# Kernel tuning notes

Measured on AMD Instinct MI355X. Metric: run time of the kernel, lower is better.

Reference implementation:

```python
import jax, jax.numpy as jnp
import numpy as np
import math

B, T, C = 1, 2048, 2048
N_HEAD = 32
N_QUERY_GROUPS = 8
HEAD_SIZE = 64
ROPE_N_ELEM = 16  # int(0.25 * 64)
Q_PER_KV = N_HEAD // N_QUERY_GROUPS  # 4
QKV_DIM = (N_HEAD + 2 * N_QUERY_GROUPS) * HEAD_SIZE  # 3072


def setup_inputs() -> dict:
    key = jax.random.key(0)
    ks = jax.random.split(key, 7)
    x = jax.random.normal(ks[0], (B, T, C), dtype=jnp.float32)
    # realistic rope tables
    inv_freq = 1.0 / (10000.0 ** (jnp.arange(0, ROPE_N_ELEM, 2, dtype=jnp.float32) / ROPE_N_ELEM))
    t = jnp.arange(T, dtype=jnp.float32)
    freqs = jnp.outer(t, inv_freq)                       # [T, rope/2]
    emb = jnp.concatenate([freqs, freqs], axis=-1)       # [T, rope]
    cos, sin = jnp.cos(emb), jnp.sin(emb)
    s = 0.02
    W_attn = jax.random.normal(ks[1], (QKV_DIM, C), dtype=jnp.float32) * s
    b_attn = jax.random.normal(ks[2], (QKV_DIM,), dtype=jnp.float32) * s
    W_proj = jax.random.normal(ks[3], (C, N_HEAD * HEAD_SIZE), dtype=jnp.float32) * s
    b_proj = jax.random.normal(ks[4], (C,), dtype=jnp.float32) * s
    return {"x": x, "cos": cos, "sin": sin, "W_attn": W_attn, "b_attn": b_attn,
            "W_proj": W_proj, "b_proj": b_proj}


def _apply_rope(t, cos, sin):
    # t: [B, H, T, rope]; cos/sin: [T, rope]
    half = t.shape[-1] // 2
    t1, t2 = t[..., :half], t[..., half:]
    rotated = jnp.concatenate([-t2, t1], axis=-1)
    return t * cos + rotated * sin


def reference(x, cos, sin, W_attn, b_attn, W_proj, b_proj):
    Bc, Tc, Cc = x.shape
    qkv = x @ W_attn.T + b_attn                                   # [B, T, 3072]
    qkv = qkv.reshape(Bc, Tc, N_QUERY_GROUPS, Q_PER_KV + 2, HEAD_SIZE)
    qkv = qkv.transpose(0, 2, 3, 1, 4)                            # [B, G, q_per_kv+2, T, hs]
    q = qkv[:, :, :Q_PER_KV]                                      # [B, G, q_per_kv, T, hs]
    k = qkv[:, :, Q_PER_KV:Q_PER_KV + 1]                          # [B, G, 1, T, hs]
    v = qkv[:, :, Q_PER_KV + 1:]
    # GQA expand (n_query_groups != n_head, prefill path)
    k = jnp.broadcast_to(k, (Bc, N_QUERY_GROUPS, Q_PER_KV, Tc, HEAD_SIZE))
    v = jnp.broadcast_to(v, (Bc, N_QUERY_GROUPS, Q_PER_KV, Tc, HEAD_SIZE))
    q = q.reshape(Bc, N_HEAD, Tc, HEAD_SIZE)
    k = k.reshape(Bc, N_HEAD, Tc, HEAD_SIZE)
    v = v.reshape(Bc, N_HEAD, Tc, HEAD_SIZE)
    # partial RoPE on first ROPE_N_ELEM dims
    q = jnp.concatenate([_apply_rope(q[..., :ROPE_N_ELEM], cos, sin), q[..., ROPE_N_ELEM:]], axis=-1)
    k = jnp.concatenate([_apply_rope(k[..., :ROPE_N_ELEM], cos, sin), k[..., ROPE_N_ELEM:]], axis=-1)
    # causal SDPA with scale 1/sqrt(head_size)
    scale = 1.0 / math.sqrt(HEAD_SIZE)
    scores = jnp.einsum('bhqd,bhkd->bhqk', q, k) * scale          # [B, H, T, T]
    causal = jnp.tril(jnp.ones((Tc, Tc), dtype=bool))
    scores = jnp.where(causal, scores, jnp.finfo(scores.dtype).min)
    attn = jax.nn.softmax(scores, axis=-1)
    y = jnp.einsum('bhqk,bhkd->bhqd', attn, v)                    # [B, H, T, hs]
    y = y.transpose(0, 2, 1, 3).reshape(Bc, Tc, N_HEAD * HEAD_SIZE)
    return y @ W_proj.T + b_proj
```

## Files before the change

kernel.cpp:

```cpp
#include <hip/hip_runtime.h>
#include <hip/hip_bf16.h>

using u16 = unsigned short;
typedef float f32x4 __attribute__((ext_vector_type(4)));
typedef __bf16 bf16x8 __attribute__((ext_vector_type(8)));

#define T_SEQ 2048
#define C_DIM 2048
#define QKV_DIM 3072
#define N_HEAD 32
#define N_GROUPS 8
#define HEAD_SIZE 64
#define ROPE_N 16
#define NEG_BIG (-1e30f)
#define LS 72
#define LSP 76
#define QSCALE 0.18033688011112043f

__device__ inline float bf2f(u16 u) {
    union { float f; unsigned v; } x; x.v = ((unsigned)u) << 16; return x.f;
}
__device__ inline u16 f2bf(float f) {
    __bf16 h = (__bf16)f;
    return *(u16*)&h;
}
__device__ inline int4 cvt8(int4 lo, int4 hi) {
    const float* fa = (const float*)&lo;
    const float* fb = (const float*)&hi;
    __attribute__((aligned(16))) u16 o[8] = {
        f2bf(fa[0]), f2bf(fa[1]), f2bf(fa[2]), f2bf(fa[3]),
        f2bf(fb[0]), f2bf(fb[1]), f2bf(fb[2]), f2bf(fb[3]) };
    return *(const int4*)o;
}

__device__ __forceinline__ int detect_fp32(const unsigned* __restrict__ xw) {
    int cnt = 0;
#pragma unroll
    for (int i = 0; i < 128; i++) {
        unsigned w = xw[i];
        cnt += (((w >> 7)  & 0xFF) >= 0xC0);
        cnt += (((w >> 23) & 0xFF) >= 0xC0);
    }
    return cnt > 8;
}

__device__ __forceinline__ void gl_lds16(const u16* g, u16* l) {
    __builtin_amdgcn_global_load_lds(
        (const __attribute__((address_space(1))) unsigned int*)g,
        (__attribute__((address_space(3))) unsigned int*)l,
        16, 0, 0);
}

struct ConvDesc {
    const void* src[7];
    u16*        dst[7];
    int         off8[8];
};

__global__ void convert_all(ConvDesc cd)
{
    const int fl = detect_fp32((const unsigned*)cd.src[0]);
    int gid = blockIdx.x * blockDim.x + threadIdx.x;
    if (gid >= cd.off8[7]) return;
    int seg = 0;
#pragma unroll
    for (int s = 1; s < 7; s++) seg += (gid >= cd.off8[s]);
    int i = (gid - cd.off8[seg]) * 8;
    if (fl) {
        const float4* s = (const float4*)((const float*)cd.src[seg] + i);
        *(int4*)(cd.dst[seg] + i) = cvt8(*(const int4*)&s[0], *(const int4*)&s[1]);
    } else {
        *(int4*)(cd.dst[seg] + i) = *(const int4*)((const u16*)cd.src[seg] + i);
    }
}

__global__ __launch_bounds__(256) void gemm_qkv_rope(
    const u16* __restrict__ A, const u16* __restrict__ W,
    const u16* __restrict__ bias,
    const u16* __restrict__ ccos, const u16* __restrict__ csin,
    u16* __restrict__ Qout, u16* __restrict__ Kout, u16* __restrict__ Vtout)
{
    __shared__ __attribute__((aligned(16))) u16 lds_a[2][64 * 64];
    __shared__ __attribute__((aligned(16))) u16 lds_b[2][128 * 64];

    const int tid  = threadIdx.x;
    const int wave = tid >> 6;
    const int lane = tid & 63;
    const int quad = lane >> 4;
    const int l16  = lane & 15;
    const int bm = blockIdx.y * 64;
    const int bn = blockIdx.x * 128;
    const int K = C_DIM;

    f32x4 acc[4][2] = {};

    int srow[4], sgc[4];
#pragma unroll
    for (int k = 0; k < 4; k++) {
        int s = tid + k * 256;
        srow[k] = s >> 3;
        sgc[k]  = (s & 7) ^ (srow[k] & 7);
    }
    const int xh = l16 & 7;

    auto stage = [&](int k0, int p) {
#pragma unroll
        for (int k = 0; k < 2; k++) {
            int s = tid + k * 256;
            gl_lds16(A + (size_t)(bm + srow[k]) * K + k0 + sgc[k] * 8, lds_a[p] + s * 8);
        }
#pragma unroll
        for (int k = 0; k < 4; k++) {
            int s = tid + k * 256;
            gl_lds16(W + (size_t)(bn + srow[k]) * K + k0 + sgc[k] * 8, lds_b[p] + s * 8);
        }
    };

    stage(0, 0);
    const int nsteps = K / 64;
    for (int kt = 0; kt < nsteps; kt++) {
        const int p = kt & 1;
        __syncthreads();
        if (kt + 1 < nsteps) stage((kt + 1) * 64, p ^ 1);

        bf16x8 afr[4][2], bfr[2][2];
#pragma unroll
        for (int ks = 0; ks < 2; ks++) {
            int c = ((ks * 4 + quad) ^ xh) * 8;
#pragma unroll
            for (int i = 0; i < 4; i++)
                afr[i][ks] = *(const bf16x8*)(lds_a[p] + (i * 16 + l16) * 64 + c);
#pragma unroll
            for (int j = 0; j < 2; j++)
                bfr[j][ks] = *(const bf16x8*)(lds_b[p] + (wave * 32 + j * 16 + l16) * 64 + c);
        }
#pragma unroll
        for (int ks = 0; ks < 2; ks++)
#pragma unroll
            for (int i = 0; i < 4; i++)
#pragma unroll
                for (int j = 0; j < 2; j++)
                    acc[i][j] = __builtin_amdgcn_mfma_f32_16x16x32_bf16(afr[i][ks], bfr[j][ks], acc[i][j], 0, 0, 0);
    }

#pragma unroll
    for (int j = 0; j < 2; j++) {
        const int colb = bn + wave * 32 + j * 16;
        const int col  = colb + l16;
        const int slot = (colb % 384) >> 6;
        const int g    = colb / 384;
        const int dbase = colb & 63;
        const int d    = dbase + l16;
        const float bv = bf2f(bias[col]);
        const bool rope = (dbase == 0) && (slot != 5);
#pragma unroll
        for (int i = 0; i < 4; i++) {
            const int trow = bm + i * 16 + quad * 4;
#pragma unroll
            for (int r = 0; r < 4; r++) {
                float v = acc[i][j][r] + bv;
                float outv = v;
                if (rope) {
                    float part = __shfl_xor(v, 8, 64);
                    float rot = (l16 < 8) ? -part : part;
                    float cc = bf2f(ccos[(trow + r) * ROPE_N + l16]);
                    float ss = bf2f(csin[(trow + r) * ROPE_N + l16]);
                    outv = v * cc + rot * ss;
                }
                const int t = trow + r;
                if (slot < 4) {
                    int hh = g * 4 + slot;
                    Qout[((size_t)hh * T_SEQ + t) * 64 + d] = f2bf(outv * QSCALE);
                } else if (slot == 4) {
                    Kout[((size_t)g * T_SEQ + t) * 64 + d] = f2bf(outv);
                } else {
                    Vtout[((size_t)g * 64 + d) * T_SEQ + t] = f2bf(outv);
                }
            }
        }
    }
}

__global__ __launch_bounds__(256) void gemm_bt(
    const u16* __restrict__ A, const u16* __restrict__ W,
    const u16* __restrict__ bias, u16* __restrict__ Cout,
    int M, int N, int K, const unsigned* __restrict__ xprobe)
{
    __shared__ __attribute__((aligned(16))) u16 lds_a[2][64 * 64];
    __shared__ __attribute__((aligned(16))) u16 lds_b[2][64 * 64];

    const int tid  = threadIdx.x;
    const int wave = tid >> 6;
    const int lane = tid & 63;
    const int quad = lane >> 4;
    const int l16  = lane & 15;
    const int bm = blockIdx.y * 64;
    const int bn = blockIdx.x * 64;
    const int fl = detect_fp32(xprobe);

    f32x4 acc[4] = {};

    int srow[2], sgc[2];
#pragma unroll
    for (int k = 0; k < 2; k++) {
        int s = tid + k * 256;
        srow[k] = s >> 3;
        sgc[k]  = (s & 7) ^ (srow[k] & 7);
    }
    const int xh = l16 & 7;

    auto stage = [&](int k0, int p) {
#pragma unroll
        for (int k = 0; k < 2; k++) {
            int s = tid + k * 256;
            gl_lds16(A + (size_t)(bm + srow[k]) * K + k0 + sgc[k] * 8, lds_a[p] + s * 8);
            gl_lds16(W + (size_t)(bn + srow[k]) * K + k0 + sgc[k] * 8, lds_b[p] + s * 8);
        }
    };

    stage(0, 0);
    const int nsteps = K / 64;
    for (int kt = 0; kt < nsteps; kt++) {
        const int p = kt & 1;
        __syncthreads();
        if (kt + 1 < nsteps) stage((kt + 1) * 64, p ^ 1);

        bf16x8 afr[4][2], bfr[2];
#pragma unroll
        for (int ks = 0; ks < 2; ks++) {
            int c = ((ks * 4 + quad) ^ xh) * 8;
#pragma unroll
            for (int i = 0; i < 4; i++)
                afr[i][ks] = *(const bf16x8*)(lds_a[p] + (i * 16 + l16) * 64 + c);
            bfr[ks] = *(const bf16x8*)(lds_b[p] + (wave * 16 + l16) * 64 + c);
        }
#pragma unroll
        for (int ks = 0; ks < 2; ks++)
#pragma unroll
            for (int i = 0; i < 4; i++)
                acc[i] = __builtin_amdgcn_mfma_f32_16x16x32_bf16(afr[i][ks], bfr[ks], acc[i], 0, 0, 0);
    }

    const int col = bn + wave * 16 + l16;
    const float bv = bf2f(bias[col]);
#pragma unroll
    for (int i = 0; i < 4; i++) {
        int row = bm + i * 16 + quad * 4;
#pragma unroll
        for (int r = 0; r < 4; r++) {
            float v = acc[i][r] + bv;
            size_t idx = (size_t)(row + r) * N + col;
            if (fl) ((float*)Cout)[idx] = v;
            else    Cout[idx] = f2bf(v);
        }
    }
}

__global__ __launch_bounds__(256) void flash_attn(
    const u16* __restrict__ Q, const u16* __restrict__ K,
    const u16* __restrict__ Vt, u16* __restrict__ Y)
{
    __shared__ __attribute__((aligned(16))) u16 lds_q[64 * LS];
    __shared__ __attribute__((aligned(16))) u16 lds_k[2][64 * LS];
    __shared__ __attribute__((aligned(16))) u16 lds_vt[2][64 * LS];
    __shared__ __attribute__((aligned(16))) u16 lds_p[4][16 * LSP];

    const int h  = blockIdx.y;
    const int g  = h >> 2;
    const int tid  = threadIdx.x;
    const int wave = tid >> 6;
    const int lane = tid & 63;
    const int quad = lane >> 4;
    const int l16  = lane & 15;
    const int NQT = T_SEQ / 64;

    const u16* Qh = Q  + (size_t)h * T_SEQ * 64;
    const u16* Kg = K  + (size_t)g * T_SEQ * 64;
    const u16* Vg = Vt + (size_t)g * 64 * T_SEQ;

    const int srow = tid >> 3, scc = (tid & 7) * 8;

    bf16x8 vones;
#pragma unroll
    for (int i = 0; i < 8; i++) vones[i] = (__bf16)1.0f;

    int4 kr0, kr1, vr0, vr1;
    auto load_tile = [&](int k0) {
        kr0 = *(const int4*)(Kg + (size_t)(k0 + srow) * 64 + scc);
        kr1 = *(const int4*)(Kg + (size_t)(k0 + srow + 32) * 64 + scc);
        vr0 = *(const int4*)(Vg + (size_t)srow * T_SEQ + k0 + scc);
        vr1 = *(const int4*)(Vg + (size_t)(srow + 32) * T_SEQ + k0 + scc);
    };

    for (int pass = 0; pass < 2; pass++) {
        const int qt = pass ? (NQT - 1 - blockIdx.x) : blockIdx.x;
        const int q0 = qt * 64;

        __syncthreads();
        for (int s = tid; s < 512; s += 256) {
            int row = s >> 3, cc = (s & 7) * 8;
            *(int4*)(lds_q + row * LS + cc) =
                *(const int4*)(Qh + (size_t)(q0 + row) * 64 + cc);
        }
        __syncthreads();

        bf16x8 a_q[2];
#pragma unroll
        for (int ks = 0; ks < 2; ks++)
            a_q[ks] = *(const bf16x8*)(lds_q + (wave * 16 + l16) * LS + ks * 32 + quad * 8);

        f32x4 o_acc[4] = {};
        f32x4 acc_l = {};

        load_tile(0);

        for (int kt = 0; kt <= qt; kt++) {
            const int p = kt & 1;
            *(int4*)(lds_k[p]  + srow * LS + scc)        = kr0;
            *(int4*)(lds_k[p]  + (srow + 32) * LS + scc) = kr1;
            *(int4*)(lds_vt[p] + srow * LS + scc)        = vr0;
            *(int4*)(lds_vt[p] + (srow + 32) * LS + scc) = vr1;
            __syncthreads();
            if (kt < qt) load_tile((kt + 1) * 64);

            f32x4 sc[4] = {};
#pragma unroll
            for (int ks = 0; ks < 2; ks++)
#pragma unroll
                for (int t = 0; t < 4; t++) {
                    bf16x8 bk = *(const bf16x8*)(lds_k[p] + (t * 16 + l16) * LS + ks * 32 + quad * 8);
                    sc[t] = __builtin_amdgcn_mfma_f32_16x16x32_bf16(a_q[ks], bk, sc[t], 0, 0, 0);
                }

            if (kt == qt) {
                const int row_g = q0 + wave * 16 + quad * 4;
                const int k0 = kt * 64;
#pragma unroll
                for (int t = 0; t < 4; t++) {
                    int col_g = k0 + t * 16 + l16;
#pragma unroll
                    for (int r = 0; r < 4; r++)
                        if (col_g > row_g + r) sc[t][r] = NEG_BIG;
                }
            }

#pragma unroll
            for (int t = 0; t < 4; t++) {
                int colo = t * 16 + l16;
#pragma unroll
                for (int r = 0; r < 4; r++) {
                    float pv = __builtin_amdgcn_exp2f(sc[t][r]);
                    lds_p[wave][(quad * 4 + r) * LSP + colo] = f2bf(pv);
                }
            }

#pragma unroll
            for (int ks = 0; ks < 2; ks++) {
                bf16x8 apf = *(const bf16x8*)(lds_p[wave] + l16 * LSP + ks * 32 + quad * 8);
#pragma unroll
                for (int t = 0; t < 4; t++) {
                    bf16x8 bvf = *(const bf16x8*)(lds_vt[p] + (t * 16 + l16) * LS + ks * 32 + quad * 8);
                    o_acc[t] = __builtin_amdgcn_mfma_f32_16x16x32_bf16(apf, bvf, o_acc[t], 0, 0, 0);
                }
                acc_l = __builtin_amdgcn_mfma_f32_16x16x32_bf16(apf, vones, acc_l, 0, 0, 0);
            }
        }

#pragma unroll
        for (int t = 0; t < 4; t++)
#pragma unroll
            for (int r = 0; r < 4; r++) {
                int row = q0 + wave * 16 + quad * 4 + r;
                int d   = t * 16 + l16;
                Y[(size_t)row * (N_HEAD * HEAD_SIZE) + h * 64 + d] = f2bf(o_acc[t][r] / acc_l[r]);
            }
    }
}

extern "C" void kernel_launch(void* const* d_in, const int* in_sizes, int n_in,
                              void* d_out, int out_size, void* d_ws, size_t ws_size,
                              hipStream_t stream)
{
    u16* base = (u16*)d_ws;

    u16* cx   = base;
    u16* cWa  = cx  + (size_t)T_SEQ * C_DIM;
    u16* cba  = cWa + (size_t)QKV_DIM * C_DIM;
    u16* cWp  = cba + QKV_DIM;
    u16* cbp  = cWp + (size_t)C_DIM * C_DIM;
    u16* ccos = cbp + C_DIM;
    u16* csin = ccos + (size_t)T_SEQ * ROPE_N;
    u16* Qb   = csin + (size_t)T_SEQ * ROPE_N;
    u16* Kb   = Qb + (size_t)N_HEAD * T_SEQ * HEAD_SIZE;
    u16* Vtb  = Kb + (size_t)N_GROUPS * T_SEQ * HEAD_SIZE;
    u16* Yb   = Vtb + (size_t)N_GROUPS * T_SEQ * HEAD_SIZE;

    dim3 blk(256);

    ConvDesc cd;
    const int sizes[7] = { T_SEQ * C_DIM, T_SEQ * ROPE_N, T_SEQ * ROPE_N,
                           QKV_DIM * C_DIM, QKV_DIM, C_DIM * C_DIM, C_DIM };
    u16* dsts[7] = { cx, ccos, csin, cWa, cba, cWp, cbp };
    int acc8 = 0;
    for (int i = 0; i < 7; i++) {
        cd.src[i] = d_in[i];
        cd.dst[i] = dsts[i];
        cd.off8[i] = acc8;
        acc8 += sizes[i] / 8;
    }
    cd.off8[7] = acc8;
    convert_all<<<dim3((acc8 + 255) / 256), blk, 0, stream>>>(cd);

    gemm_qkv_rope<<<dim3(QKV_DIM / 128, T_SEQ / 64), blk, 0, stream>>>(
        cx, cWa, cba, ccos, csin, Qb, Kb, Vtb);
    flash_attn<<<dim3(T_SEQ / 128, N_HEAD), blk, 0, stream>>>(Qb, Kb, Vtb, Yb);
    gemm_bt<<<dim3(C_DIM / 64, T_SEQ / 64), blk, 0, stream>>>(
        Yb, cWp, cbp, (u16*)d_out, T_SEQ, C_DIM, N_HEAD * HEAD_SIZE,
        (const unsigned*)d_in[0]);
}
```

Measured before the change: 251.0 us.

## Use direct global-to-LDS async loads with XOR swizzle in flash attention

The flash attention kernel now stages Q, K and V tiles straight into shared memory with a gl_lds16 helper (presumably defined in the hidden part of the file) instead of going through registers. Padded rows are replaced by an XOR-swizzled layout to avoid bank conflicts. The two-pass causal pairing per block becomes one query tile per block, launched longest-first over twice as many blocks. This aims to cut register pressure and load latency, at the cost of losing the paired load balancing, and it depends on the async LDS load semantics and barrier placement being correct.

```diff
diff --git a/kernel.cpp b/kernel.cpp
--- a/kernel.cpp
+++ b/kernel.cpp
@@ -13,7 +13,6 @@
 #define HEAD_SIZE 64
 #define ROPE_N 16
 #define NEG_BIG (-1e30f)
-#define LS 72
 #define LSP 76
 #define QSCALE 0.18033688011112043f
 
@@ -260,121 +259,125 @@
     const u16* __restrict__ Q, const u16* __restrict__ K,
     const u16* __restrict__ Vt, u16* __restrict__ Y)
 {
-    __shared__ __attribute__((aligned(16))) u16 lds_q[64 * LS];
-    __shared__ __attribute__((aligned(16))) u16 lds_k[2][64 * LS];
-    __shared__ __attribute__((aligned(16))) u16 lds_vt[2][64 * LS];
+    __shared__ __attribute__((aligned(16))) u16 lds_q[64 * 64];
+    __shared__ __attribute__((aligned(16))) u16 lds_k[2][64 * 64];
+    __shared__ __attribute__((aligned(16))) u16 lds_vt[2][64 * 64];
     __shared__ __attribute__((aligned(16))) u16 lds_p[4][16 * LSP];
 
     const int h  = blockIdx.y;
     const int g  = h >> 2;
+    const int qt = 31 - blockIdx.x;
+    const int q0 = qt * 64;
     const int tid  = threadIdx.x;
     const int wave = tid >> 6;
     const int lane = tid & 63;
     const int quad = lane >> 4;
     const int l16  = lane & 15;
-    const int NQT = T_SEQ / 64;
 
     const u16* Qh = Q  + (size_t)h * T_SEQ * 64;
     const u16* Kg = K  + (size_t)g * T_SEQ * 64;
     const u16* Vg = Vt + (size_t)g * 64 * T_SEQ;
 
-    const int srow = tid >> 3, scc = (tid & 7) * 8;
+    int srow[2], sgc[2];
+#pragma unroll
+    for (int k = 0; k < 2; k++) {
+        int s = tid + k * 256;
+        srow[k] = s >> 3;
+        sgc[k]  = (s & 7) ^ (srow[k] & 7);
+    }
+    const int xh = l16 & 7;
 
     bf16x8 vones;
 #pragma unroll
     for (int i = 0; i < 8; i++) vones[i] = (__bf16)1.0f;
 
-    int4 kr0, kr1, vr0, vr1;
-    auto load_tile = [&](int k0) {
-        kr0 = *(const int4*)(Kg + (size_t)(k0 + srow) * 64 + scc);
-        kr1 = *(const int4*)(Kg + (size_t)(k0 + srow + 32) * 64 + scc);
-        vr0 = *(const int4*)(Vg + (size_t)srow * T_SEQ + k0 + scc);
-        vr1 = *(const int4*)(Vg + (size_t)(srow + 32) * T_SEQ + k0 + scc);
+    auto stage = [&](int k0, int p) {
+#pragma unroll
+        for (int k = 0; k < 2; k++) {
+            int s = tid + k * 256;
+            gl_lds16(Kg + (size_t)(k0 + srow[k]) * 64 + sgc[k] * 8, lds_k[p] + s * 8);
+            gl_lds16(Vg + (size_t)srow[k] * T_SEQ + k0 + sgc[k] * 8, lds_vt[p] + s * 8);
+        }
     };
 
-    for (int pass = 0; pass < 2; pass++) {
-        const int qt = pass ? (NQT - 1 - blockIdx.x) : blockIdx.x;
-        const int q0 = qt * 64;
-
+#pragma unroll
+    for (int k = 0; k < 2; k++) {
+        int s = tid + k * 256;
+        gl_lds16(Qh + (size_t)(q0 + srow[k]) * 64 + sgc[k] * 8, lds_q + s * 8);
+    }
+    stage(0, 0);
+
+    f32x4 o_acc[4] = {};
+    f32x4 acc_l = {};
+    bf16x8 a_q[2];
+    bool q_loaded = false;
+
+    for (int kt = 0; kt <= qt; kt++) {
+        const int p = kt & 1;
         __syncthreads();
-        for (int s = tid; s < 512; s += 256) {
-            int row = s >> 3, cc = (s & 7) * 8;
-            *(int4*)(lds_q + row * LS + cc) =
-                *(const int4*)(Qh + (size_t)(q0 + row) * 64 + cc);
-        }
-        __syncthreads();
-
-        bf16x8 a_q[2];
-#pragma unroll
-        for (int ks = 0; ks < 2; ks++)
-            a_q[ks] = *(const bf16x8*)(lds_q + (wave * 16 + l16) * LS + ks * 32 + quad * 8);
-
-        f32x4 o_acc[4] = {};
-        f32x4 acc_l = {};
-
-        load_tile(0);
-
-        for (int kt = 0; kt <= qt; kt++) {
-            const int p = kt & 1;
-            *(int4*)(lds_k[p]  + srow * LS + scc)        = kr0;
-            *(int4*)(lds_k[p]  + (srow + 32) * LS + scc) = kr1;
-            *(int4*)(lds_vt[p] + srow * LS + scc)        = vr0;
-            *(int4*)(lds_vt[p] + (srow + 32) * LS + scc) = vr1;
-            __syncthreads();
-            if (kt < qt) load_tile((kt + 1) * 64);
-
-            f32x4 sc[4] = {};
+        if (kt < qt) stage((kt + 1) * 64, p ^ 1);
+
+        if (!q_loaded) {
 #pragma unroll
             for (int ks = 0; ks < 2; ks++)
-#pragma unroll
-                for (int t = 0; t < 4; t++) {
-                    bf16x8 bk = *(const bf16x8*)(lds_k[p] + (t * 16 + l16) * LS + ks * 32 + quad * 8);
-                    sc[t] = __builtin_amdgcn_mfma_f32_16x16x32_bf16(a_q[ks], bk, sc[t], 0, 0, 0);
-                }
-
-            if (kt == qt) {
-                const int row_g = q0 + wave * 16 + quad * 4;
-                const int k0 = kt * 64;
-#pragma unroll
-                for (int t = 0; t < 4; t++) {
-                    int col_g = k0 + t * 16 + l16;
-#pragma unroll
-                    for (int r = 0; r < 4; r++)
-                        if (col_g > row_g + r) sc[t][r] = NEG_BIG;
-                }
+                a_q[ks] = *(const bf16x8*)(lds_q + (wave * 16 + l16) * 64 + (((ks * 4 + quad) ^ xh) * 8));
+            q_loaded = true;
+        }
+
+        f32x4 sc[4] = {};
+#pragma unroll
+        for (int ks = 0; ks < 2; ks++) {
+            int c = ((ks * 4 + quad) ^ xh) * 8;
+#pragma unroll
+            for (int t = 0; t < 4; t++) {
+                bf16x8 bk = *(const bf16x8*)(lds_k[p] + (t * 16 + l16) * 64 + c);
+                sc[t] = __builtin_amdgcn_mfma_f32_16x16x32_bf16(a_q[ks], bk, sc[t], 0, 0, 0);
             }
-
+        }
+
+        if (kt == qt) {
+            const int row_g = q0 + wave * 16 + quad * 4;
+            const int k0 = kt * 64;
 #pragma unroll
             for (int t = 0; t < 4; t++) {
-                int colo = t * 16 + l16;
-#pragma unroll
-                for (int r = 0; r < 4; r++) {
-                    float pv = __builtin_amdgcn_exp2f(sc[t][r]);
-                    lds_p[wave][(quad * 4 + r) * LSP + colo] = f2bf(pv);
-                }
+                int col_g = k0 + t * 16 + l16;
+#pragma unroll
+                for (int r = 0; r < 4; r++)
+                    if (col_g > row_g + r) sc[t][r] = NEG_BIG;
             }
-
-#pragma unroll
-            for (int ks = 0; ks < 2; ks++) {
-                bf16x8 apf = *(const bf16x8*)(lds_p[wave] + l16 * LSP + ks * 32 + quad * 8);
-#pragma unroll
-                for (int t = 0; t < 4; t++) {
-                    bf16x8 bvf = *(const bf16x8*)(lds_vt[p] + (t * 16 + l16) * LS + ks * 32 + quad * 8);
-                    o_acc[t] = __builtin_amdgcn_mfma_f32_16x16x32_bf16(apf, bvf, o_acc[t], 0, 0, 0);
-                }
-                acc_l = __builtin_amdgcn_mfma_f32_16x16x32_bf16(apf, vones, acc_l, 0, 0, 0);
+        }
+
+#pragma unroll
+        for (int t = 0; t < 4; t++) {
+            int colo = t * 16 + l16;
+#pragma unroll
+            for (int r = 0; r < 4; r++) {
+                float pv = __builtin_amdgcn_exp2f(sc[t][r]);
+                lds_p[wave][(quad * 4 + r) * LSP + colo] = f2bf(pv);
             }
         }
 
 #pragma unroll
-        for (int t = 0; t < 4; t++)
-#pragma unroll
-            for (int r = 0; r < 4; r++) {
-                int row = q0 + wave * 16 + quad * 4 + r;
-                int d   = t * 16 + l16;
-                Y[(size_t)row * (N_HEAD * HEAD_SIZE) + h * 64 + d] = f2bf(o_acc[t][r] / acc_l[r]);
+        for (int ks = 0; ks < 2; ks++) {
+            int c = ((ks * 4 + quad) ^ xh) * 8;
+            bf16x8 apf = *(const bf16x8*)(lds_p[wave] + l16 * LSP + ks * 32 + quad * 8);
+#pragma unroll
+            for (int t = 0; t < 4; t++) {
+                bf16x8 bvf = *(const bf16x8*)(lds_vt[p] + (t * 16 + l16) * 64 + c);
+                o_acc[t] = __builtin_amdgcn_mfma_f32_16x16x32_bf16(apf, bvf, o_acc[t], 0, 0, 0);
             }
-    }
+            acc_l = __builtin_amdgcn_mfma_f32_16x16x32_bf16(apf, vones, acc_l, 0, 0, 0);
+        }
+    }
+
+#pragma unroll
+    for (int t = 0; t < 4; t++)
+#pragma unroll
+        for (int r = 0; r < 4; r++) {
+            int row = q0 + wave * 16 + quad * 4 + r;
+            int d   = t * 16 + l16;
+            Y[(size_t)row * (N_HEAD * HEAD_SIZE) + h * 64 + d] = f2bf(o_acc[t][r] / acc_l[r]);
+        }
 }
 
 extern "C" void kernel_launch(void* const* d_in, const int* in_sizes, int n_in,
@@ -413,7 +416,7 @@
 
     gemm_qkv_rope<<<dim3(QKV_DIM / 128, T_SEQ / 64), blk, 0, stream>>>(
         cx, cWa, cba, ccos, csin, Qb, Kb, Vtb);
-    flash_attn<<<dim3(T_SEQ / 128, N_HEAD), blk, 0, stream>>>(Qb, Kb, Vtb, Yb);
+    flash_attn<<<dim3(T_SEQ / 64, N_HEAD), blk, 0, stream>>>(Qb, Kb, Vtb, Yb);
     gemm_bt<<<dim3(C_DIM / 64, T_SEQ / 64), blk, 0, stream>>>(
         Yb, cWp, cbp, (u16*)d_out, T_SEQ, C_DIM, N_HEAD * HEAD_SIZE,
         (const unsigned*)d_in[0]);
```

New measurement: 281.5 us. +12.1%, slower.
